# Kernel tuning notes

Measured on AMD Instinct MI355X. Metric: run time of the kernel, lower is better.

Reference implementation:

```python
import jax, jax.numpy as jnp
import numpy as np

B, N, E, H, TOP_K = 2, 2048, 1024, 16, 64
Dh = E // H


def _linear_init(k, fan_in, shape):
    bound = 1.0 / np.sqrt(fan_in)
    return jax.random.uniform(k, shape, jnp.float32, -bound, bound)


def setup_inputs() -> dict:
    key = jax.random.key(0)
    ks = jax.random.split(key, 11)
    return {
        "query": jax.random.normal(ks[0], (B, N, E), jnp.float32),
        "key": jax.random.normal(ks[1], (B, N, E), jnp.float32),
        "value": jax.random.normal(ks[2], (B, N, E), jnp.float32),
        "Wq": _linear_init(ks[3], E, (E, E)),
        "bq": _linear_init(ks[4], E, (E,)),
        "Wk": _linear_init(ks[5], E, (E, E)),
        "bk": _linear_init(ks[6], E, (E,)),
        "Wv": _linear_init(ks[7], E, (E, E)),
        "bv": _linear_init(ks[8], E, (E,)),
        "Wo": _linear_init(ks[9], E, (E, E)),
        "bo": _linear_init(ks[10], E, (E,)),
    }


def _split_heads(x):
    # (B, N, E) -> (B*H, N, Dh)
    return x.reshape(B, N, H, Dh).transpose(0, 2, 1, 3).reshape(B * H, N, Dh)


def _merge_heads(x):
    # (B*H, N, Dh) -> (B, N, E)
    return x.reshape(B, H, N, Dh).transpose(0, 2, 1, 3).reshape(B, N, E)


def _topk_attention(q, k, v, top_k):
    # q,k,v: (BH, N, Dh). Faithful to _classical_efficient_attention:
    # scores scaled by sqrt(last dim of Q) == sqrt(Dh).
    scores = jnp.einsum("bqd,bkd->bqk", q, k) / jnp.sqrt(jnp.float32(q.shape[-1]))
    top_scores, top_idx = jax.lax.top_k(scores, min(top_k, scores.shape[-1]))
    w = jax.nn.softmax(top_scores, axis=-1)  # (BH, Nq, K)
    # gather V rows: (BH, 1, Nk, Dh) indexed along axis 2 -> (BH, Nq, K, Dh)
    vals = jnp.take_along_axis(v[:, None, :, :], top_idx[..., None], axis=2)
    return jnp.einsum("bqk,bqkd->bqd", w, vals)


def reference(query, key, value, Wq, bq, Wk, bk, Wv, bv, Wo, bo):
    q = _split_heads(query @ Wq.T + bq)
    k = _split_heads(key @ Wk.T + bk)
    v = _split_heads(value @ Wv.T + bv)
    out = _topk_attention(q, k, v, TOP_K)
    return _merge_heads(out) @ Wo.T + bo
```

## Files before the change

kernel.cpp:

```cpp
#include <hip/hip_runtime.h>
#include <stdint.h>
#include <math.h>

#define Bk 2
#define Nk 2048
#define Ek 1024
#define Hk 16
#define DHk 64
#define BLENDW 5e-5
#define PRECAND 96
#define CANDCAP 128

using short8 = __attribute__((ext_vector_type(8))) short;
using f32x4  = __attribute__((ext_vector_type(4))) float;

__device__ __forceinline__ unsigned short bf16rne(float f) {
    const unsigned u = __float_as_uint(f);
    return (unsigned short)((u + 0x7FFFu + ((u >> 16) & 1u)) >> 16);
}

__global__ __launch_bounds__(256) void cvt_split(
    const float* __restrict__ in, unsigned short* __restrict__ oh,
    unsigned short* __restrict__ ol)
{
    const int i = blockIdx.x * 256 + threadIdx.x;
    const float4 a = ((const float4*)in)[i * 2];
    const float4 b = ((const float4*)in)[i * 2 + 1];
    float x[8] = {a.x, a.y, a.z, a.w, b.x, b.y, b.z, b.w};
    unsigned short hs[8], ls[8];
#pragma unroll
    for (int j = 0; j < 8; ++j) {
        hs[j] = bf16rne(x[j]);
        const float hf = __uint_as_float((unsigned)hs[j] << 16);
        ls[j] = bf16rne(x[j] - hf);
    }
    uint4 ho, lo;
    ho.x = hs[0] | ((unsigned)hs[1] << 16); ho.y = hs[2] | ((unsigned)hs[3] << 16);
    ho.z = hs[4] | ((unsigned)hs[5] << 16); ho.w = hs[6] | ((unsigned)hs[7] << 16);
    lo.x = ls[0] | ((unsigned)ls[1] << 16); lo.y = ls[2] | ((unsigned)ls[3] << 16);
    lo.z = ls[4] | ((unsigned)ls[5] << 16); lo.w = ls[6] | ((unsigned)ls[7] << 16);
    ((uint4*)oh)[i] = ho;
    ((uint4*)ol)[i] = lo;
}

template<int MODE>
__global__ __launch_bounds__(256, 4) void gemm_mfma(
    const unsigned short* __restrict__ Xh, const unsigned short* __restrict__ Xl,
    const unsigned short* __restrict__ Wh, const unsigned short* __restrict__ Wl,
    const float* __restrict__ bias, float* __restrict__ out,
    unsigned short* __restrict__ obf)
{
    __shared__ unsigned short Ah[128][40], Al[128][40];
    __shared__ unsigned short Bh[64][40],  Bl[64][40];

    const int tid  = threadIdx.x;
    const int lane = tid & 63;
    const int wv   = tid >> 6;
    const int n16  = lane & 15;
    const int quad = lane >> 4;
    const int mBase = blockIdx.y * 128;
    const int nBase = blockIdx.x * 64;

    f32x4 acc[2][4];
#pragma unroll
    for (int i = 0; i < 2; ++i)
#pragma unroll
        for (int j = 0; j < 4; ++j) acc[i][j] = (f32x4){0.f, 0.f, 0.f, 0.f};

    const int arow = tid >> 1, aoff = (tid & 1) * 16;
    const int brow = tid >> 2, boff = (tid & 3) * 8;
    const size_t aIdx = (size_t)(mBase + arow) * Ek + aoff;
    const size_t bIdx = (size_t)(nBase + brow) * Ek + boff;

    for (int kt = 0; kt < Ek; kt += 32) {
        const uint4 ah0 = *(const uint4*)(Xh + aIdx + kt);
        const uint4 ah1 = *(const uint4*)(Xh + aIdx + kt + 8);
        const uint4 al0 = *(const uint4*)(Xl + aIdx + kt);
        const uint4 al1 = *(const uint4*)(Xl + aIdx + kt + 8);
        const uint4 bh0 = *(const uint4*)(Wh + bIdx + kt);
        const uint4 bl0 = *(const uint4*)(Wl + bIdx + kt);
        __syncthreads();
        *(uint4*)&Ah[arow][aoff]     = ah0;
        *(uint4*)&Ah[arow][aoff + 8] = ah1;
        *(uint4*)&Al[arow][aoff]     = al0;
        *(uint4*)&Al[arow][aoff + 8] = al1;
        *(uint4*)&Bh[brow][boff]     = bh0;
        *(uint4*)&Bl[brow][boff]     = bl0;
        __syncthreads();

        const short8 fa_h0 = *(const short8*)&Ah[wv*32 +      n16][quad*8];
        const short8 fa_l0 = *(const short8*)&Al[wv*32 +      n16][quad*8];
        const short8 fa_h1 = *(const short8*)&Ah[wv*32 + 16 + n16][quad*8];
        const short8 fa_l1 = *(const short8*)&Al[wv*32 + 16 + n16][quad*8];
#pragma unroll
        for (int ct = 0; ct < 4; ++ct) {
            const short8 fb_h = *(const short8*)&Bh[ct*16 + n16][quad*8];
            const short8 fb_l = *(const short8*)&Bl[ct*16 + n16][quad*8];
            acc[0][ct] = __builtin_amdgcn_mfma_f32_16x16x32_bf16(fa_h0, fb_h, acc[0][ct], 0, 0, 0);
            acc[0][ct] = __builtin_amdgcn_mfma_f32_16x16x32_bf16(fa_h0, fb_l, acc[0][ct], 0, 0, 0);
            acc[0][ct] = __builtin_amdgcn_mfma_f32_16x16x32_bf16(fa_l0, fb_h, acc[0][ct], 0, 0, 0);
            acc[1][ct] = __builtin_amdgcn_mfma_f32_16x16x32_bf16(fa_h1, fb_h, acc[1][ct], 0, 0, 0);
            acc[1][ct] = __builtin_amdgcn_mfma_f32_16x16x32_bf16(fa_h1, fb_l, acc[1][ct], 0, 0, 0);
            acc[1][ct] = __builtin_amdgcn_mfma_f32_16x16x32_bf16(fa_l1, fb_h, acc[1][ct], 0, 0, 0);
        }
    }

#pragma unroll
    for (int mt = 0; mt < 2; ++mt)
#pragma unroll
    for (int ct = 0; ct < 4; ++ct) {
        const int c  = nBase + ct*16 + n16;
        const float bv = bias[c];
#pragma unroll
        for (int reg = 0; reg < 4; ++reg) {
            const int m = mBase + wv*32 + mt*16 + quad*4 + reg;
            const float o = acc[mt][ct][reg] + bv;
            size_t dst;
            if (MODE == 0) {
                dst = (size_t)m * Ek + c;
            } else {
                const int bb = m >> 11, nn = m & 2047;
                const int hh = c >> 6,  dd = c & 63;
                dst = (((size_t)(bb*Hk + hh) * Nk) + nn) * DHk + dd;
            }
            out[dst] = o;
            if (MODE == 1 && obf) obf[dst] = bf16rne(o);
        }
    }
}

__device__ __forceinline__ unsigned fkey(float s) {
    const unsigned b = __float_as_uint(s);
    return (b & 0x80000000u) ? ~b : (b | 0x80000000u);
}
__device__ __forceinline__ unsigned long long dkey(double s) {
    unsigned long long b = (unsigned long long)__double_as_longlong(s);
    return (b & 0x8000000000000000ull) ? ~b : (b | 0x8000000000000000ull);
}
__device__ __forceinline__ double dinv(unsigned long long u) {
    const unsigned long long b =
        (u & 0x8000000000000000ull) ? (u & 0x7fffffffffffffffull) : ~u;
    return __longlong_as_double((long long)b);
}

__device__ __forceinline__ int dpp_wsum_i32(int x) {
#define STEP(C) x += __builtin_amdgcn_update_dpp(0, x, C, 0xf, 0xf, true);
    STEP(0x111) STEP(0x112) STEP(0x114) STEP(0x118) STEP(0x142) STEP(0x143)
#undef STEP
    return __builtin_amdgcn_readlane(x, 63);
}
__device__ __forceinline__ float dpp_wsum_f32(float x) {
#define STEP(C) { const int t_ = __builtin_amdgcn_update_dpp(0, __float_as_int(x), C, 0xf, 0xf, true); \
                  x += __int_as_float(t_); }
    STEP(0x111) STEP(0x112) STEP(0x114) STEP(0x118) STEP(0x142) STEP(0x143)
#undef STEP
    return __int_as_float(__builtin_amdgcn_readlane(__float_as_int(x), 63));
}
__device__ __forceinline__ float dpp_wmax_f32(float x) {
#define STEP(C) { const int t_ = __builtin_amdgcn_update_dpp(__float_as_int(x), __float_as_int(x), C, 0xf, 0xf, false); \
                  x = fmaxf(x, __int_as_float(t_)); }
    STEP(0x111) STEP(0x112) STEP(0x114) STEP(0x118) STEP(0x142) STEP(0x143)
#undef STEP
    return __int_as_float(__builtin_amdgcn_readlane(__float_as_int(x), 63));
}
__device__ __forceinline__ unsigned dpp_wmin_u32(unsigned x) {
#define STEP(C) { const unsigned t_ = (unsigned)__builtin_amdgcn_update_dpp((int)x, (int)x, C, 0xf, 0xf, false); \
                  x = x < t_ ? x : t_; }
    STEP(0x111) STEP(0x112) STEP(0x114) STEP(0x118) STEP(0x142) STEP(0x143)
#undef STEP
    return (unsigned)__builtin_amdgcn_readlane((int)x, 63);
}
__device__ __forceinline__ unsigned dpp_wmax_u32(unsigned x) {
#define STEP(C) { const unsigned t_ = (unsigned)__builtin_amdgcn_update_dpp((int)x, (int)x, C, 0xf, 0xf, false); \
                  x = x > t_ ? x : t_; }
    STEP(0x111) STEP(0x112) STEP(0x114) STEP(0x118) STEP(0x142) STEP(0x143)
#undef STEP
    return (unsigned)__builtin_amdgcn_readlane((int)x, 63);
}
__device__ __forceinline__ int dpp_wprefix_incl_i32(int x) {
    x += __builtin_amdgcn_update_dpp(0, x, 0x111, 0xf, 0xf, true);
    x += __builtin_amdgcn_update_dpp(0, x, 0x112, 0xf, 0xf, true);
    x += __builtin_amdgcn_update_dpp(0, x, 0x114, 0xf, 0xf, true);
    x += __builtin_amdgcn_update_dpp(0, x, 0x118, 0xf, 0xf, true);
    x += __builtin_amdgcn_update_dpp(0, x, 0x142, 0xa, 0xf, true);
    x += __builtin_amdgcn_update_dpp(0, x, 0x143, 0xc, 0xf, true);
    return x;
}

__device__ __forceinline__ void proc_row(
    const int lane, const int lrow,
    unsigned s0, unsigned s1, unsigned s2, unsigned s3,
    unsigned s4, unsigned s5, unsigned s6, unsigned s7,
    unsigned s8, unsigned s9, unsigned s10, unsigned s11,
    unsigned s12, unsigned s13, unsigned s14, unsigned s15,
    const float* __restrict__ Kb, const float (*qsf)[68],
    unsigned long long (*ck)[CANDCAP], unsigned (*ci)[CANDCAP],
    unsigned long long (*wvi)[64], unsigned (*eq_idx)[64],
    int& i65_out, float& lam_out)
{
    const unsigned long long lmask = (1ull << lane) - 1ull;

    const unsigned q0 = s0 << 16,  q1 = s1 << 16,  q2 = s2 << 16,  q3 = s3 << 16;
    const unsigned q4 = s4 << 16,  q5 = s5 << 16,  q6 = s6 << 16,  q7 = s7 << 16;
    const unsigned q8 = s8 << 16,  q9 = s9 << 16,  q10 = s10 << 16, q11 = s11 << 16;
    const unsigned q12 = s12 << 16, q13 = s13 << 16, q14 = s14 << 16, q15 = s15 << 16;

    unsigned m1 = 0u, m2 = 0u;
#define T2(V) { const unsigned t_ = (V) < m1 ? (V) : m1; \
                m1 = m1 > (V) ? m1 : (V);  m2 = m2 > t_ ? m2 : t_; }
    T2(s0)  T2(s1)  T2(s2)  T2(s3)  T2(s4)  T2(s5)  T2(s6)  T2(s7)
    T2(s8)  T2(s9)  T2(s10) T2(s11) T2(s12) T2(s13) T2(s14) T2(s15)
    T2(q0)  T2(q1)  T2(q2)  T2(q3)  T2(q4)  T2(q5)  T2(q6)  T2(q7)
    T2(q8)  T2(q9)  T2(q10) T2(q11) T2(q12) T2(q13) T2(q14) T2(q15)
#undef T2
    unsigned lo16 = dpp_wmin_u32(m2) >> 16;
    unsigned hi16 = dpp_wmax_u32(m1) >> 16;

    while (lo16 < hi16) {
        const unsigned mid = lo16 + ((hi16 - lo16) >> 1) + 1u;
        const unsigned M = mid << 16;
        int c0 = 0, c1 = 0, c2 = 0, c3 = 0;
        c0 += (s0  >= M); c0 += (q0  >= M); c0 += (s1  >= M); c0 += (q1  >= M);
        c0 += (s2  >= M); c0 += (q2  >= M); c0 += (s3  >= M); c0 += (q3  >= M);
        c1 += (s4  >= M); c1 += (q4  >= M); c1 += (s5  >= M); c1 += (q5  >= M);
        c1 += (s6  >= M); c1 += (q6  >= M); c1 += (s7  >= M); c1 += (q7  >= M);
        c2 += (s8  >= M); c2 += (q8  >= M); c2 += (s9  >= M); c2 += (q9  >= M);
        c2 += (s10 >= M); c2 += (q10 >= M); c2 += (s11 >= M); c2 += (q11 >= M);
        c3 += (s12 >= M); c3 += (q12 >= M); c3 += (s13 >= M); c3 += (q13 >= M);
        c3 += (s14 >= M); c3 += (q14 >= M); c3 += (s15 >= M); c3 += (q15 >= M);
        const int c = dpp_wsum_i32((c0 + c1) + (c2 + c3));
        if (c >= PRECAND) {
            lo16 = mid;
            if (c <= CANDCAP) break;
        } else hi16 = mid - 1u;
    }
    const unsigned THsh = lo16 << 16;

    int cnt = 0;
#define CC(S, Q) { cnt += ((Q) >= THsh); cnt += ((S) >= THsh); }
    CC(s0, q0)    CC(s1, q1)    CC(s2, q2)    CC(s3, q3)
    CC(s4, q4)    CC(s5, q5)    CC(s6, q6)    CC(s7, q7)
    CC(s8, q8)    CC(s9, q9)    CC(s10, q10)  CC(s11, q11)
    CC(s12, q12)  CC(s13, q13)  CC(s14, q14)  CC(s15, q15)
#undef CC
    const int incl = dpp_wprefix_incl_i32(cnt);
    int pos = incl - cnt;
    int nc = __builtin_amdgcn_readlane(incl, 63);
    if (nc > CANDCAP) nc = CANDCAP;
#define CE(W, S, Q) { \
        if ((Q) >= THsh) { \
            if (pos < CANDCAP) \
                ci[lrow][pos] = (unsigned)((((W) >> 2) * 512) + (((W) & 3) * 128) + 2 * lane); \
            ++pos; } \
        if ((S) >= THsh) { \
            if (pos < CANDCAP) \
                ci[lrow][pos] = (unsigned)((((W) >> 2) * 512) + (((W) & 3) * 128) + 2 * lane + 1); \
            ++pos; } }
    CE(0, s0, q0)     CE(1, s1, q1)     CE(2, s2, q2)     CE(3, s3, q3)
    CE(4, s4, q4)     CE(5, s5, q5)     CE(6, s6, q6)     CE(7, s7, q7)
    CE(8, s8, q8)     CE(9, s9, q9)     CE(10, s10, q10)  CE(11, s11, q11)
    CE(12, s12, q12)  CE(13, s13, q13)  CE(14, s14, q14)  CE(15, s15, q15)
#undef CE

    const int c8 = lane >> 3, d8 = lane & 7;
    const float* qrow = &qsf[lrow][d8 * 8];
    const double qd0 = (double)qrow[0], qd1 = (double)qrow[1];
    const double qd2 = (double)qrow[2], qd3 = (double)qrow[3];
    const double qd4 = (double)qrow[4], qd5 = (double)qrow[5];
    const double qd6 = (double)qrow[6], qd7 = (double)qrow[7];
    const int nb = (nc + 7) >> 3;
    for (int b = 0; b < nb; ++b) {
        const int s  = b * 8 + c8;
        const int s2 = s < nc ? s : nc - 1;
        const unsigned cidx = ci[lrow][s2];
        const unsigned kb32 = (cidx << 6) + (unsigned)(d8 * 8);
        const float2 kv0 = *(const float2*)(Kb + kb32);
        const float2 kv1 = *(const float2*)(Kb + kb32 + 2);
        const float2 kv2 = *(const float2*)(Kb + kb32 + 4);
        const float2 kv3 = *(const float2*)(Kb + kb32 + 6);
        double acc = 0.0;
        acc = fma(qd0, (double)kv0.x, acc);
        acc = fma(qd1, (double)kv0.y, acc);
        acc = fma(qd2, (double)kv1.x, acc);
        acc = fma(qd3, (double)kv1.y, acc);
        acc = fma(qd4, (double)kv2.x, acc);
        acc = fma(qd5, (double)kv2.y, acc);
        acc = fma(qd6, (double)kv3.x, acc);
        acc = fma(qd7, (double)kv3.y, acc);
        acc += __shfl_xor(acc, 1);
        acc += __shfl_xor(acc, 2);
        acc += __shfl_xor(acc, 4);
        if (d8 == 0 && s < nc) ck[lrow][s] = dkey(acc * 0.125);
    }

    const unsigned long long k0 = (lane      < nc) ? ck[lrow][lane]      : 0ull;
    const unsigned long long k1 = (lane + 64 < nc) ? ck[lrow][lane + 64] : 0ull;
    const unsigned idx0 = ci[lrow][lane];
    const unsigned idx1 = ci[lrow][(lane + 64) & (CANDCAP - 1)];
    const unsigned kh0 = (unsigned)(k0 >> 32), kh1 = (unsigned)(k1 >> 32);
    const unsigned kl0 = (unsigned)k0,         kl1 = (unsigned)k1;

    unsigned H;
    {
        const unsigned i0 = (k0 != 0ull) ? kh0 : 0xFFFFFFFFu;
        const unsigned i1 = (k1 != 0ull) ? kh1 : 0xFFFFFFFFu;
        unsigned lo = dpp_wmin_u32(i0 < i1 ? i0 : i1);
        unsigned hi = dpp_wmax_u32(kh0 > kh1 ? kh0 : kh1);
        bool done = false;
        while (lo < hi) {
            const unsigned mid = lo + ((hi - lo) >> 1) + 1u;
            const int c = __popcll(__ballot(kh0 >= mid))
                        + __popcll(__ballot(kh1 >= mid));
            if (c == 64) {
                const unsigned v0 = (kh0 >= mid) ? kh0 : 0xFFFFFFFFu;
                const unsigned v1 = (kh1 >= mid) ? kh1 : 0xFFFFFFFFu;
                H = dpp_wmin_u32(v0 < v1 ? v0 : v1);
                done = true; break;
            }
            if (c >= 64) lo = mid; else hi = mid - 1u;
        }
        if (!done) H = lo;
    }
    const int cGtHi = __popcll(__ballot(kh0 > H))
                    + __popcll(__ballot(kh1 > H));
    const int need1 = 64 - cGtHi;

    const bool e0v = (kh0 == H) && (k0 != 0ull);
    const bool e1v = (kh1 == H) && (k1 != 0ull);
    const int cEq = __popcll(__ballot(e0v)) + __popcll(__ballot(e1v));
    unsigned Tlo;
    if (need1 == cEq) {
        const unsigned v0 = e0v ? kl0 : 0xFFFFFFFFu;
        const unsigned v1 = e1v ? kl1 : 0xFFFFFFFFu;
        Tlo = dpp_wmin_u32(v0 < v1 ? v0 : v1);
    } else if (need1 == 1) {
        const unsigned v0 = e0v ? kl0 : 0u;
        const unsigned v1 = e1v ? kl1 : 0u;
        Tlo = dpp_wmax_u32(v0 > v1 ? v0 : v1);
    } else {
        unsigned lo = 0u, hi = 0xFFFFFFFFu;
        bool done = false;
        while (lo < hi) {
            const unsigned mid = lo + ((hi - lo) >> 1) + 1u;
            const int c = __popcll(__ballot(e0v && kl0 >= mid))
                        + __popcll(__ballot(e1v && kl1 >= mid));
            if (c == need1) {
                const unsigned v0 = (e0v && kl0 >= mid) ? kl0 : 0xFFFFFFFFu;
                const unsigned v1 = (e1v && kl1 >= mid) ? kl1 : 0xFFFFFFFFu;
                Tlo = dpp_wmin_u32(v0 < v1 ? v0 : v1);
                done = true; break;
            }
            if (c >= need1) lo = mid; else hi = mid - 1u;
        }
        if (!done) Tlo = lo;
    }
    const unsigned long long T = ((unsigned long long)H << 32) | Tlo;

    int base = 0;
    {
        const bool g0 = k0 > T;
        unsigned long long m = __ballot(g0);
        if (g0) {
            const int pos2 = base + __popcll(m & lmask);
            wvi[lrow][pos2] = ((unsigned long long)__float_as_uint((float)dinv(k0)) << 32)
                            | (unsigned long long)idx0;
        }
        base += __popcll(m);
        const bool g1 = k1 > T;
        m = __ballot(g1);
        if (g1) {
            const int pos2 = base + __popcll(m & lmask);
            wvi[lrow][pos2] = ((unsigned long long)__float_as_uint((float)dinv(k1)) << 32)
                            | (unsigned long long)idx1;
        }
        base += __popcll(m);
    }

    int ne = 0;
    {
        const bool e0 = k0 == T;
        unsigned long long m = __ballot(e0);
        if (e0) {
            const int pos2 = ne + __popcll(m & lmask);
            if (pos2 < 64) eq_idx[lrow][pos2] = idx0;
        }
        ne += __popcll(m);
        const bool e1 = k1 == T;
        m = __ballot(e1);
        if (e1) {
            const int pos2 = ne + __popcll(m & lmask);
            if (pos2 < 64) eq_idx[lrow][pos2] = idx1;
        }
        ne += __popcll(m);
    }
    if (ne > 64) ne = 64;

    const int   need = 64 - base;
    const float tvf  = (float)dinv(T);
    if (lane < need) {
        unsigned my = 0u;
        for (int j = 0; j < ne; ++j) {
            const unsigned v = eq_idx[lrow][j];
            int rank = 0;
            for (int j2 = 0; j2 < ne; ++j2) rank += (eq_idx[lrow][j2] < v) ? 1 : 0;
            if (rank == lane) my = v;
        }
        wvi[lrow][base + lane] = ((unsigned long long)__float_as_uint(tvf) << 32)
                               | (unsigned long long)my;
    }

    unsigned long long m2k = 0ull;
    if (k0 < T && k0 > m2k) m2k = k0;
    if (k1 < T && k1 > m2k) m2k = k1;
#pragma unroll
    for (int off = 32; off > 0; off >>= 1) {
        const unsigned long long o =
            (unsigned long long)__shfl_xor((long long)m2k, off);
        if (o > m2k) m2k = o;
    }
    int i65 = 0;
    {
        unsigned long long mm = __ballot(k0 == m2k && m2k != 0ull);
        if (mm) i65 = __shfl((int)idx0, (int)(__ffsll((long long)mm) - 1));
        else {
            mm = __ballot(k1 == m2k && m2k != 0ull);
            if (mm) i65 = __shfl((int)idx1, (int)(__ffsll((long long)mm) - 1));
        }
    }
    double fr = (dinv(T) - dinv(m2k)) * (1.0 / BLENDW);
    if (fr > 1.0) fr = 1.0;
    i65_out = i65;
    lam_out = (m2k == 0ull) ? 0.f : (float)(0.5 * (1.0 - fr));
}

__global__ __launch_bounds__(1024, 8) void attn_topk_mfma(
    const float* __restrict__ qf, const float* __restrict__ kf,
    const unsigned short* __restrict__ kbf,
    const float* __restrict__ vh, float* __restrict__ outm)
{
    __shared__ __align__(16) char uS[33024];
    float (*sc)[516] = (float(*)[516])uS;
    unsigned long long (*ck)[CANDCAP] = (unsigned long long(*)[CANDCAP])uS;
    unsigned (*ci)[CANDCAP] = (unsigned(*)[CANDCAP])(uS + 16384);

    __shared__ float          qsf[16][68];
    __shared__ unsigned short qbf[16][72];
    __shared__ unsigned long long wvi[16][64];
    __shared__ unsigned eq_idx[16][64];

    const int tid  = threadIdx.x;
    const int lane = tid & 63;
    const int wv   = tid >> 6;

    const int wid  = (blockIdx.x & 7) * 512 + (blockIdx.x >> 3);
    const int slot = wid >> 7;
    const int qt   = wid & 127;
    const int bb   = slot >> 4;
    const int hh   = slot & 15;

    const float*          Qb = qf  + (size_t)slot * Nk * DHk + (size_t)qt * 16 * DHk;
    const float*          Kb = kf  + (size_t)slot * Nk * DHk;
    const unsigned short* KB = kbf + (size_t)slot * Nk * DHk;
    const float*          Vb = vh  + (size_t)slot * Nk * DHk;

    {
        const int r = tid >> 6, d = tid & 63;
        const float qv = Qb[r * DHk + d];
        qsf[r][d] = qv;
        qbf[r][d] = bf16rne(qv);
    }
    __syncthreads();

    const int n16  = lane & 15;
    const int quad = lane >> 4;
    short8 afrag0, afrag1;
    afrag0 = *(const short8*)&qbf[n16][quad * 8];
    afrag1 = *(const short8*)&qbf[n16][32 + quad * 8];

    unsigned p0, p1, p2, p3, p4, p5, p6, p7;
    unsigned p8, p9, p10, p11, p12, p13, p14, p15;
    const int rowD = quad * 4;

#define QK_TILE(CH, T, ACC) { \
    const unsigned short* kp = KB + ((size_t)(CH) * 512 + (wv * 2 + (T)) * 16 + n16) * DHk + quad * 8; \
    const short8 b0_ = *(const short8*)(kp); \
    const short8 b1_ = *(const short8*)(kp + 32); \
    ACC = __builtin_amdgcn_mfma_f32_16x16x32_bf16(afrag0, b0_, ACC, 0, 0, 0); \
    ACC = __builtin_amdgcn_mfma_f32_16x16x32_bf16(afrag1, b1_, ACC, 0, 0, 0); \
}
#define SC_STORE(T, ACC) { \
    const int ccol = (wv * 2 + (T)) * 16 + n16; \
    sc[rowD + 0][ccol] = ACC[0]; sc[rowD + 1][ccol] = ACC[1]; \
    sc[rowD + 2][ccol] = ACC[2]; sc[rowD + 3][ccol] = ACC[3]; \
}
#define PACKW(J, DEST) { \
    const float2 pr_ = *(const float2*)&sc[wv][(J) * 128 + 2 * lane]; \
    DEST = (fkey(pr_.x) >> 16) | ((fkey(pr_.y) >> 16) << 16); \
}
#define DO_CHUNK(CH, D0, D1, D2, D3) { \
    f32x4 ac0 = {0.f,0.f,0.f,0.f}, ac1 = {0.f,0.f,0.f,0.f}; \
    QK_TILE(CH, 0, ac0) QK_TILE(CH, 1, ac1) \
    __syncthreads();                    \
    SC_STORE(0, ac0) SC_STORE(1, ac1) \
    __syncthreads(); \
    PACKW(0, D0) PACKW(1, D1) PACKW(2, D2) PACKW(3, D3) \
}
    DO_CHUNK(0, p0,  p1,  p2,  p3)
    DO_CHUNK(1, p4,  p5,  p6,  p7)
    DO_CHUNK(2, p8,  p9,  p10, p11)
    DO_CHUNK(3, p12, p13, p14, p15)
#undef DO_CHUNK
#undef PACKW
#undef SC_STORE
#undef QK_TILE

    __syncthreads();

    int i65_0; float lam_0;
    proc_row(lane, wv,
             p0, p1, p2, p3, p4, p5, p6, p7,
             p8, p9, p10, p11, p12, p13, p14, p15,
             Kb, qsf, ck, ci, wvi, eq_idx, i65_0, lam_0);

    {
        const unsigned long long e = wvi[wv][lane];
        const float    sv = __uint_as_float((unsigned)(e >> 32));
        const unsigned vi = (unsigned)e;
        const float mx = dpp_wmax_f32(sv);
        const float p  = __expf(sv - mx);
        const float Z  = dpp_wsum_f32(p);
        const float w  = p / Z;
        wvi[wv][lane] = ((unsigned long long)__float_as_uint(w) << 32)
                      | (unsigned long long)vi;

        float acc = 0.f;
#pragma unroll
        for (int j = 0; j < 64; ++j) {
            const unsigned long long ej = wvi[wv][j];
            const float wj = __uint_as_float((unsigned)(ej >> 32));
            const unsigned ij = (unsigned)ej;
            acc = fmaf(wj, Vb[(ij << 6) + (unsigned)lane], acc);
        }
        {
            const unsigned long long e63 = wvi[wv][63];
            const float    wT  = __uint_as_float((unsigned)(e63 >> 32));
            const unsigned i64 = (unsigned)e63;
            acc += wT * lam_0 *
                   (Vb[((unsigned)i65_0 << 6) + (unsigned)lane]
                  - Vb[(i64 << 6) + (unsigned)lane]);
        }
        const int gq = qt * 16 + wv;
        outm[((size_t)bb * Nk + gq) * Ek + hh * DHk + lane] = acc;
    }
}

extern "C" void kernel_launch(void* const* d_in, const int* in_sizes, int n_in,
                              void* d_out, int out_size, void* d_ws, size_t ws_size,
                              hipStream_t stream)
{
    const float* query = (const float*)d_in[0];
    const float* key   = (const float*)d_in[1];
    const float* value = (const float*)d_in[2];
    const float* Wq    = (const float*)d_in[3];
    const float* bq    = (const float*)d_in[4];
    const float* Wk    = (const float*)d_in[5];
    const float* bk    = (const float*)d_in[6];
    const float* Wv    = (const float*)d_in[7];
    const float* bv    = (const float*)d_in[8];
    const float* Wo    = (const float*)d_in[9];
    const float* bo    = (const float*)d_in[10];
    float* out = (float*)d_out;
    (void)in_sizes; (void)n_in; (void)out_size; (void)ws_size;

    const size_t seg  = (size_t)(Bk * Hk) * Nk * DHk;
    const size_t wseg = (size_t)Ek * Ek;
    float* qfp = (float*)d_ws;
    float* kfp = qfp + seg;
    float* vws = kfp + seg;
    float* aws = vws + seg;
    unsigned short* kbf = (unsigned short*)(aws + seg);
    unsigned short* xh  = kbf + seg;
    unsigned short* xl  = xh + seg;
    unsigned short* wh  = xl + seg;
    unsigned short* wl  = wh + wseg;

    const dim3 blk(256);
    const dim3 gG(16, 32);
    const int  gX = (int)(seg  / 2048);
    const int  gW = (int)(wseg / 2048);

    hipLaunchKernelGGL(cvt_split, dim3(gX), blk, 0, stream, query, xh, xl);
    hipLaunchKernelGGL(cvt_split, dim3(gW), blk, 0, stream, Wq, wh, wl);
    hipLaunchKernelGGL((gemm_mfma<1>), gG, blk, 0, stream, xh, xl, wh, wl, bq, qfp, (unsigned short*)nullptr);
    hipLaunchKernelGGL(cvt_split, dim3(gX), blk, 0, stream, key, xh, xl);
    hipLaunchKernelGGL(cvt_split, dim3(gW), blk, 0, stream, Wk, wh, wl);
    hipLaunchKernelGGL((gemm_mfma<1>), gG, blk, 0, stream, xh, xl, wh, wl, bk, kfp, kbf);
    hipLaunchKernelGGL(cvt_split, dim3(gX), blk, 0, stream, value, xh, xl);
    hipLaunchKernelGGL(cvt_split, dim3(gW), blk, 0, stream, Wv, wh, wl);
    hipLaunchKernelGGL((gemm_mfma<1>), gG, blk, 0, stream, xh, xl, wh, wl, bv, vws, (unsigned short*)nullptr);
    hipLaunchKernelGGL(attn_topk_mfma, dim3(32 * 128), dim3(1024), 0, stream,
                       qfp, kfp, kbf, vws, aws);
    hipLaunchKernelGGL(cvt_split, dim3(gX), blk, 0, stream, aws, xh, xl);
    hipLaunchKernelGGL(cvt_split, dim3(gW), blk, 0, stream, Wo, wh, wl);
    hipLaunchKernelGGL((gemm_mfma<0>), gG, blk, 0, stream, xh, xl, wh, wl, bo, out, (unsigned short*)nullptr);
}
```

Before: 580.9 us.

## Store K bf16 in MFMA fragment-major layout and use DPP max for runner-up

The projection epilogue now writes the bf16 copy of K in a tiled layout where each 16-row by 64-dim tile is stored fragment-major, so a wave's B-fragment loads in the QK tile become fully contiguous 16-byte-per-lane reads. The QK loader address is updated to match. Separately, the 64-bit runner-up score search is replaced by two 32-bit DPP wave max reductions instead of a six-step 64-bit shuffle loop. Risk lies in consistency between the writer's swizzle and the reader's indexing, and the epilogue's bf16 stores become more scattered.

After: 560.0 us. -3.6%, faster.

```diff
diff --git a/kernel.cpp b/kernel.cpp
--- a/kernel.cpp
+++ b/kernel.cpp
@@ -115,16 +115,21 @@
         for (int reg = 0; reg < 4; ++reg) {
             const int m = mBase + wv*32 + mt*16 + quad*4 + reg;
             const float o = acc[mt][ct][reg] + bv;
-            size_t dst;
             if (MODE == 0) {
-                dst = (size_t)m * Ek + c;
+                out[(size_t)m * Ek + c] = o;
             } else {
-                const int bb = m >> 11, nn = m & 2047;
-                const int hh = c >> 6,  dd = c & 63;
-                dst = (((size_t)(bb*Hk + hh) * Nk) + nn) * DHk + dd;
+                const int bb2 = m >> 11, nn = m & 2047;
+                const int hh2 = c >> 6,  dd = c & 63;
+                const size_t sb = (size_t)(bb2*Hk + hh2) * Nk * DHk;
+                out[sb + (size_t)nn * DHk + dd] = o;
+                if (obf) {
+                    const size_t kdst = sb + (size_t)(nn >> 4) * 1024
+                                      + ((dd >> 5) * 512)
+                                      + ((((dd >> 3) & 3) * 16 + (nn & 15)) * 8)
+                                      + (dd & 7);
+                    obf[kdst] = bf16rne(o);
+                }
             }
-            out[dst] = o;
-            if (MODE == 1 && obf) obf[dst] = bf16rne(o);
         }
     }
 }
@@ -313,8 +318,8 @@
                         + __popcll(__ballot(kh1 >= mid));
             if (c == 64) {
                 const unsigned v0 = (kh0 >= mid) ? kh0 : 0xFFFFFFFFu;
-                const unsigned v1 = (kh1 >= mid) ? kh1 : 0xFFFFFFFFu;
-                H = dpp_wmin_u32(v0 < v1 ? v0 : v1);
+                const unsigned v1m = (kh1 >= mid) ? kh1 : 0xFFFFFFFFu;
+                H = dpp_wmin_u32(v0 < v1m ? v0 : v1m);
                 done = true; break;
             }
             if (c >= 64) lo = mid; else hi = mid - 1u;
@@ -331,12 +336,12 @@
     unsigned Tlo;
     if (need1 == cEq) {
         const unsigned v0 = e0v ? kl0 : 0xFFFFFFFFu;
-        const unsigned v1 = e1v ? kl1 : 0xFFFFFFFFu;
-        Tlo = dpp_wmin_u32(v0 < v1 ? v0 : v1);
+        const unsigned v1m = e1v ? kl1 : 0xFFFFFFFFu;
+        Tlo = dpp_wmin_u32(v0 < v1m ? v0 : v1m);
     } else if (need1 == 1) {
         const unsigned v0 = e0v ? kl0 : 0u;
-        const unsigned v1 = e1v ? kl1 : 0u;
-        Tlo = dpp_wmax_u32(v0 > v1 ? v0 : v1);
+        const unsigned v1m = e1v ? kl1 : 0u;
+        Tlo = dpp_wmax_u32(v0 > v1m ? v0 : v1m);
     } else {
         unsigned lo = 0u, hi = 0xFFFFFFFFu;
         bool done = false;
@@ -346,8 +351,8 @@
                         + __popcll(__ballot(e1v && kl1 >= mid));
             if (c == need1) {
                 const unsigned v0 = (e0v && kl0 >= mid) ? kl0 : 0xFFFFFFFFu;
-                const unsigned v1 = (e1v && kl1 >= mid) ? kl1 : 0xFFFFFFFFu;
-                Tlo = dpp_wmin_u32(v0 < v1 ? v0 : v1);
+                const unsigned v1m = (e1v && kl1 >= mid) ? kl1 : 0xFFFFFFFFu;
+                Tlo = dpp_wmin_u32(v0 < v1m ? v0 : v1m);
                 done = true; break;
             }
             if (c >= need1) lo = mid; else hi = mid - 1u;
@@ -409,15 +414,14 @@
                                | (unsigned long long)my;
     }
 
-    unsigned long long m2k = 0ull;
-    if (k0 < T && k0 > m2k) m2k = k0;
-    if (k1 < T && k1 > m2k) m2k = k1;
-#pragma unroll
-    for (int off = 32; off > 0; off >>= 1) {
-        const unsigned long long o =
-            (unsigned long long)__shfl_xor((long long)m2k, off);
-        if (o > m2k) m2k = o;
-    }
+    const unsigned mh0 = (k0 < T) ? kh0 : 0u;
+    const unsigned mh1 = (k1 < T) ? kh1 : 0u;
+    const unsigned Hm = dpp_wmax_u32(mh0 > mh1 ? mh0 : mh1);
+    const unsigned ml0 = (k0 < T && kh0 == Hm) ? kl0 : 0u;
+    const unsigned ml1 = (k1 < T && kh1 == Hm) ? kl1 : 0u;
+    const unsigned Lm = dpp_wmax_u32(ml0 > ml1 ? ml0 : ml1);
+    const unsigned long long m2k = ((unsigned long long)Hm << 32) | Lm;
+
     int i65 = 0;
     {
         unsigned long long mm = __ballot(k0 == m2k && m2k != 0ull);
@@ -482,9 +486,9 @@
     const int rowD = quad * 4;
 
 #define QK_TILE(CH, T, ACC) { \
-    const unsigned short* kp = KB + ((size_t)(CH) * 512 + (wv * 2 + (T)) * 16 + n16) * DHk + quad * 8; \
+    const unsigned short* kp = KB + (((CH) * 32) + (wv * 2 + (T))) * 1024 + lane * 8; \
     const short8 b0_ = *(const short8*)(kp); \
-    const short8 b1_ = *(const short8*)(kp + 32); \
+    const short8 b1_ = *(const short8*)(kp + 512); \
     ACC = __builtin_amdgcn_mfma_f32_16x16x32_bf16(afrag0, b0_, ACC, 0, 0, 0); \
     ACC = __builtin_amdgcn_mfma_f32_16x16x32_bf16(afrag1, b1_, ACC, 0, 0, 0); \
 }
```
